# Optimization experiments

Hardware: AMD Instinct MI355X
Metric: run time of the kernel (lower is better)

Reference implementation:

```python
import jax, jax.numpy as jnp
import numpy as np

# Static 4-level feature pyramid (H, W) per level; total tokens = 20197
SHAPES = [(100, 152), (50, 76), (25, 38), (13, 19)]
B, S, E, H, L, P, R = 4, 1024, 256, 8, 4, 20, 4
HD = E // H
OFFSET_SCALE = 4.0


def setup_inputs() -> dict:
    key = jax.random.key(0)
    ks = jax.random.split(key, 11)
    total = sum(h * w for h, w in SHAPES)
    s = 0.02
    return {
        "x": jax.random.normal(ks[0], (B, S, E), jnp.float32),
        "encoder_input": jax.random.normal(ks[1], (B, total, E), jnp.float32),
        "v_w": jax.random.normal(ks[2], (E, E), jnp.float32) * s,
        "out_w": jax.random.normal(ks[3], (E, E), jnp.float32) * s,
        "off_w": jax.random.normal(ks[4], (H * L * P * 2, E), jnp.float32) * s,
        "off_b": jax.random.normal(ks[5], (H * L * P * 2,), jnp.float32) * s,
        "attn_w": jax.random.normal(ks[6], (H * L * P, E), jnp.float32) * s,
        "attn_b": jax.random.normal(ks[7], (H * L * P,), jnp.float32) * s,
        "ref_w": jax.random.normal(ks[8], (H * R, E), jnp.float32) * s,
        "ref_b": jax.random.normal(ks[9], (H * R,), jnp.float32) * s,
        "def_refs": jax.random.uniform(ks[10], (R, 2), jnp.float32, 0.1, 0.9),
        "spatial_shapes": jnp.array(SHAPES, dtype=jnp.int32),
    }


def _grid_sample(img, gx, gy, Hh, Ww):
    """Bilinear grid_sample, padding_mode='zeros', align_corners=False.
    img: (N, C, Hh*Ww); gx, gy: (N, M) in [-1, 1]. Returns (N, C, M)."""
    x = ((gx + 1.0) * Ww - 1.0) * 0.5
    y = ((gy + 1.0) * Hh - 1.0) * 0.5
    x0 = jnp.floor(x)
    y0 = jnp.floor(y)
    wx = x - x0
    wy = y - y0
    x0i = x0.astype(jnp.int32)
    y0i = y0.astype(jnp.int32)
    N, C, _ = img.shape

    def gather(xi, yi):
        valid = (xi >= 0) & (xi < Ww) & (yi >= 0) & (yi < Hh)
        idx = jnp.clip(yi, 0, Hh - 1) * Ww + jnp.clip(xi, 0, Ww - 1)
        v = jnp.take_along_axis(
            img, jnp.broadcast_to(idx[:, None, :], (N, C, idx.shape[-1])), axis=2)
        return v * valid[:, None, :].astype(img.dtype)

    return (gather(x0i, y0i) * ((1 - wx) * (1 - wy))[:, None, :]
            + gather(x0i + 1, y0i) * (wx * (1 - wy))[:, None, :]
            + gather(x0i, y0i + 1) * ((1 - wx) * wy)[:, None, :]
            + gather(x0i + 1, y0i + 1) * (wx * wy)[:, None, :])


def reference(x, encoder_input, v_w, out_w, off_w, off_b, attn_w, attn_b,
              ref_w, ref_b, def_refs, spatial_shapes):
    b, s, _ = x.shape
    values = (encoder_input @ v_w.T).reshape(b, -1, H, HD)
    refs = jax.nn.sigmoid(def_refs)  # (R, 2), default reference points
    ref_mix = jax.nn.softmax((x @ ref_w.T + ref_b).reshape(b, s, H, R), axis=-1)
    anchors = jnp.einsum('bshr,rc->bshc', ref_mix, refs)  # (b, s, H, 2)
    offsets = (x @ off_w.T + off_b).reshape(b, s, H, L, P, 2)
    attn = jax.nn.softmax((x @ attn_w.T + attn_b).reshape(b, s, H, L * P),
                          axis=-1).reshape(b, s, H, L, P)

    out = jnp.zeros((b, s, H, HD), x.dtype)
    start = 0
    for lvl, (hh, ww) in enumerate(SHAPES):  # static per-level loop (L=4)
        img = values[:, start:start + hh * ww]  # (b, hh*ww, H, HD)
        start += hh * ww
        img = img.transpose(0, 2, 3, 1).reshape(b * H, HD, hh * ww)
        norm = jnp.array([max(ww, 1), max(hh, 1)], x.dtype)
        locs = anchors[:, :, :, None, :] + jnp.tanh(offsets[:, :, :, lvl]) * (OFFSET_SCALE / norm)
        grid = jnp.clip(locs, 0.0, 1.0) * 2.0 - 1.0  # (b, s, H, P, 2)
        grid = grid.transpose(0, 2, 1, 3, 4).reshape(b * H, s * P, 2)
        sampled = _grid_sample(img, grid[..., 0], grid[..., 1], hh, ww)  # (b*H, HD, s*P)
        sampled = sampled.reshape(b, H, HD, s, P)
        out = out + jnp.einsum('bhcsp,bshp->bshc', sampled, attn[:, :, :, lvl])
    return out.reshape(b, s, E) @ out_w.T
```

## Files before the change

kernel.cpp:

```cpp
#include <hip/hip_runtime.h>
#include <hip/hip_bf16.h>
#include <math.h>

#define NH 8
#define HD 32
#define EDIM 256
#define NL 4
#define NP 20
#define NR 4
#define SEQ 1024
#define BATCH 4
#define TOTAL 20197
#define OFF_SCALE 4.0f

#define M_ENC (BATCH * TOTAL)
#define M_PAD 80896
#define KDIM 256

typedef short bf16x8 __attribute__((ext_vector_type(8)));
typedef float f32x4  __attribute__((ext_vector_type(4)));

__global__ __launch_bounds__(256) void cast_f32_bf16_kernel(
    const float* __restrict__ src, unsigned short* __restrict__ dst,
    long n_src, long n_dst)
{
    long i = (long)blockIdx.x * blockDim.x + threadIdx.x;
    long stride = (long)gridDim.x * blockDim.x;
    for (long e = i * 8; e < n_dst; e += stride * 8) {
        unsigned short o[8];
        if (e < n_src) {
            float4 a = *reinterpret_cast<const float4*>(src + e);
            float4 b = *reinterpret_cast<const float4*>(src + e + 4);
            float f[8] = {a.x, a.y, a.z, a.w, b.x, b.y, b.z, b.w};
            #pragma unroll
            for (int j = 0; j < 8; ++j) {
                unsigned u = __float_as_uint(f[j]);
                o[j] = (unsigned short)((u + 0x7fffu + ((u >> 16) & 1u)) >> 16);
            }
        } else {
            #pragma unroll
            for (int j = 0; j < 8; ++j) o[j] = 0;
        }
        *reinterpret_cast<uint4*>(dst + e) = *reinterpret_cast<const uint4*>(o);
    }
}

__global__ __launch_bounds__(256) void gemm_mfma_kernel(
    const unsigned short* __restrict__ A,
    const unsigned short* __restrict__ W,
    const float* __restrict__ bias,
    float* __restrict__ C,
    int M_real, int N)
{
    __shared__ __align__(16) unsigned short As[128 * 32];
    __shared__ __align__(16) unsigned short Ws[128 * 32];

    const int tid  = threadIdx.x;
    const int m0   = blockIdx.x * 128;
    const int n0   = blockIdx.y * 128;
    const int wave = tid >> 6;
    const int lane = tid & 63;
    const int wr   = wave >> 1;
    const int wc   = wave & 1;
    const int lrow = lane & 15;
    const int kg   = lane >> 4;

    f32x4 acc[4][4] = {};

    const bf16x8* Asv = reinterpret_cast<const bf16x8*>(As);
    const bf16x8* Wsv = reinterpret_cast<const bf16x8*>(Ws);

    for (int k0 = 0; k0 < KDIM; k0 += 32) {
        #pragma unroll
        for (int it = 0; it < 2; ++it) {
            int s   = tid + it * 256;
            int row = s >> 2;
            int ks  = s & 3;
            uint4 va = *reinterpret_cast<const uint4*>(A + (size_t)(m0 + row) * KDIM + k0 + ks * 8);
            uint4 vw = *reinterpret_cast<const uint4*>(W + (size_t)(n0 + row) * KDIM + k0 + ks * 8);
            *reinterpret_cast<uint4*>(&As[s * 8]) = va;
            *reinterpret_cast<uint4*>(&Ws[s * 8]) = vw;
        }
        __syncthreads();

        bf16x8 af[4], bfr[4];
        #pragma unroll
        for (int mi = 0; mi < 4; ++mi)
            af[mi] = Asv[(wr * 64 + mi * 16 + lrow) * 4 + kg];
        #pragma unroll
        for (int nj = 0; nj < 4; ++nj)
            bfr[nj] = Wsv[(wc * 64 + nj * 16 + lrow) * 4 + kg];
        #pragma unroll
        for (int mi = 0; mi < 4; ++mi)
            #pragma unroll
            for (int nj = 0; nj < 4; ++nj)
                acc[mi][nj] = __builtin_amdgcn_mfma_f32_16x16x32_bf16(
                    af[mi], bfr[nj], acc[mi][nj], 0, 0, 0);
        __syncthreads();
    }

    #pragma unroll
    for (int mi = 0; mi < 4; ++mi) {
        #pragma unroll
        for (int nj = 0; nj < 4; ++nj) {
            int row_base = m0 + wr * 64 + mi * 16 + kg * 4;
            int col      = n0 + wc * 64 + nj * 16 + lrow;
            float bv = bias ? bias[col] : 0.f;
            #pragma unroll
            for (int r = 0; r < 4; ++r) {
                int row = row_base + r;
                if (row < M_real)
                    C[(size_t)row * N + col] = acc[mi][nj][r] + bv;
            }
        }
    }
}

__global__ __launch_bounds__(256) void gemm_atb_kernel(
    const float* __restrict__ A, const float* __restrict__ W,
    const float* __restrict__ bias, float* __restrict__ C,
    int M, int N, int K)
{
    __shared__ float As[16][64];
    __shared__ float Wt[16][64];

    const int tid = threadIdx.x;
    const int m0 = blockIdx.x * 64;
    const int n0 = blockIdx.y * 64;
    const int tx = tid & 15;
    const int ty = tid >> 4;
    const int lr = tid >> 2;
    const int lk = (tid & 3) << 2;

    const int am = m0 + lr;
    const int wn = n0 + lr;

    float acc[4][4] = {};

    for (int k0 = 0; k0 < K; k0 += 16) {
        float4 av = make_float4(0.f, 0.f, 0.f, 0.f);
        float4 wv = make_float4(0.f, 0.f, 0.f, 0.f);
        if (am < M) av = *reinterpret_cast<const float4*>(&A[(size_t)am * K + k0 + lk]);
        if (wn < N) wv = *reinterpret_cast<const float4*>(&W[(size_t)wn * K + k0 + lk]);
        As[lk + 0][lr] = av.x; As[lk + 1][lr] = av.y;
        As[lk + 2][lr] = av.z; As[lk + 3][lr] = av.w;
        Wt[lk + 0][lr] = wv.x; Wt[lk + 1][lr] = wv.y;
        Wt[lk + 2][lr] = wv.z; Wt[lk + 3][lr] = wv.w;
        __syncthreads();

        #pragma unroll
        for (int k = 0; k < 16; ++k) {
            float a[4], b[4];
            #pragma unroll
            for (int i = 0; i < 4; ++i) a[i] = As[k][ty * 4 + i];
            #pragma unroll
            for (int j = 0; j < 4; ++j) b[j] = Wt[k][tx * 4 + j];
            #pragma unroll
            for (int i = 0; i < 4; ++i)
                #pragma unroll
                for (int j = 0; j < 4; ++j)
                    acc[i][j] += a[i] * b[j];
        }
        __syncthreads();
    }

    #pragma unroll
    for (int i = 0; i < 4; ++i) {
        int m = m0 + ty * 4 + i;
        if (m >= M) continue;
        #pragma unroll
        for (int j = 0; j < 4; ++j) {
            int n = n0 + tx * 4 + j;
            if (n >= N) continue;
            float v = acc[i][j];
            if (bias) v += bias[n];
            C[(size_t)m * N + n] = v;
        }
    }
}

__global__ __launch_bounds__(256) void deform_sample_kernel(
    const float* __restrict__ values,
    const float* __restrict__ proj_off,
    const float* __restrict__ proj_attn,
    const float* __restrict__ proj_ref,
    const float* __restrict__ def_refs,
    float* __restrict__ out)
{
    const int row = blockIdx.x;
    const int b   = row >> 10;
    const int tid = threadIdx.x;

    __shared__ float  attn_s[NH * NL * NP];
    __shared__ float  anchors[NH][2];
    __shared__ unsigned int sidx[NH * NL * NP][2];
    __shared__ float4 wcor[NH * NL * NP];

    if (tid >= 96) {
        int i = tid - 96;
        reinterpret_cast<float4*>(attn_s)[i] =
            reinterpret_cast<const float4*>(proj_attn + (size_t)row * 640)[i];
    } else if (tid < NH) {
        const int h = tid;
        float rv[NR];
        float rmax = -1e30f;
        #pragma unroll
        for (int r = 0; r < NR; ++r) {
            rv[r] = proj_ref[(size_t)row * (NH * NR) + h * NR + r];
            rmax = fmaxf(rmax, rv[r]);
        }
        float rsum = 0.f;
        #pragma unroll
        for (int r = 0; r < NR; ++r) { rv[r] = __expf(rv[r] - rmax); rsum += rv[r]; }
        float ax = 0.f, ay = 0.f;
        #pragma unroll
        for (int r = 0; r < NR; ++r) {
            float pr = rv[r] / rsum;
            float sx = 1.f / (1.f + __expf(-def_refs[r * 2 + 0]));
            float sy = 1.f / (1.f + __expf(-def_refs[r * 2 + 1]));
            ax += pr * sx; ay += pr * sy;
        }
        anchors[h][0] = ax; anchors[h][1] = ay;
    }
    __syncthreads();

    {
        const int g = tid >> 5;
        const int l = tid & 31;
        float v0 = attn_s[g * 80 + l];
        float v1 = attn_s[g * 80 + 32 + l];
        float v2 = (l < 16) ? attn_s[g * 80 + 64 + l] : -1e30f;
        float m = fmaxf(fmaxf(v0, v1), v2);
        #pragma unroll
        for (int d = 16; d >= 1; d >>= 1) m = fmaxf(m, __shfl_xor(m, d, 64));
        float e0 = __expf(v0 - m), e1 = __expf(v1 - m);
        float e2 = (l < 16) ? __expf(v2 - m) : 0.f;
        float s = e0 + e1 + e2;
        #pragma unroll
        for (int d = 16; d >= 1; d >>= 1) s += __shfl_xor(s, d, 64);
        float inv = 1.f / s;
        __syncthreads();
        attn_s[g * 80 + l]      = e0 * inv;
        attn_s[g * 80 + 32 + l] = e1 * inv;
        if (l < 16) attn_s[g * 80 + 64 + l] = e2 * inv;
    }
    __syncthreads();

    const int lhh[NL] = {100, 50, 25, 13};
    const int lww[NL] = {152, 76, 38, 19};
    const int lst[NL] = {0, 15200, 19000, 19950};

    for (int e = tid; e < NH * NL * NP; e += 256) {
        int h = e / 80;
        int rem = e - h * 80;
        int l = rem / 20;
        const float2 o = *reinterpret_cast<const float2*>(
            proj_off + (size_t)row * 1280 + e * 2);
        float offx = tanhf(o.x);
        float offy = tanhf(o.y);
        int ww = lww[l], hh = lhh[l];
        float locx = fminf(fmaxf(anchors[h][0] + offx * (OFF_SCALE / (float)ww), 0.f), 1.f);
        float locy = fminf(fmaxf(anchors[h][1] + offy * (OFF_SCALE / (float)hh), 0.f), 1.f);
        float xx = locx * (float)ww - 0.5f;
        float yy = locy * (float)hh - 0.5f;
        float x0f = floorf(xx), y0f = floorf(yy);
        int x0 = (int)x0f, y0 = (int)y0f;
        float wx = xx - x0f, wy = yy - y0f;
        float wa = attn_s[e];

        float bx0 = (x0 >= 0)      ? 1.f : 0.f;
        float bx1 = (x0 < ww - 1)  ? 1.f : 0.f;
        float by0 = (y0 >= 0)      ? 1.f : 0.f;
        float by1 = (y0 < hh - 1)  ? 1.f : 0.f;
        int xc0 = max(x0, 0), xc1 = min(x0 + 1, ww - 1);
        int yc0 = max(y0, 0), yc1 = min(y0 + 1, hh - 1);
        unsigned int i00 = (unsigned int)(lst[l] + yc0 * ww + xc0);
        unsigned int i10 = (unsigned int)(lst[l] + yc0 * ww + xc1);
        unsigned int i01 = (unsigned int)(lst[l] + yc1 * ww + xc0);
        unsigned int i11 = (unsigned int)(lst[l] + yc1 * ww + xc1);

        float4 w;
        w.x = wa * (1.f - wx) * (1.f - wy) * bx0 * by0;
        w.y = wa * wx * (1.f - wy) * bx1 * by0;
        w.z = wa * (1.f - wx) * wy * bx0 * by1;
        w.w = wa * wx * wy * bx1 * by1;

        sidx[e][0] = i00 | (i10 << 16);
        sidx[e][1] = i01 | (i11 << 16);
        wcor[e] = w;
    }
    __syncthreads();

    const int h = tid >> 5;
    const int c = tid & 31;
    const float* vb = values + (size_t)b * TOTAL * 256 + h * 32 + c;
    float acc = 0.f;
    #pragma unroll 4
    for (int i = 0; i < 80; ++i) {
        int e = h * 80 + i;
        unsigned int p0 = sidx[e][0];
        unsigned int p1 = sidx[e][1];
        float4 w = wcor[e];
        float v00 = vb[(size_t)(p0 & 0xffffu) * 256];
        float v10 = vb[(size_t)(p0 >> 16) * 256];
        float v01 = vb[(size_t)(p1 & 0xffffu) * 256];
        float v11 = vb[(size_t)(p1 >> 16) * 256];
        acc += w.x * v00 + w.y * v10 + w.z * v01 + w.w * v11;
    }
    out[(size_t)row * 256 + h * 32 + c] = acc;
}

extern "C" void kernel_launch(void* const* d_in, const int* in_sizes, int n_in,
                              void* d_out, int out_size, void* d_ws, size_t ws_size,
                              hipStream_t stream)
{
    const float* x        = (const float*)d_in[0];
    const float* enc      = (const float*)d_in[1];
    const float* v_w      = (const float*)d_in[2];
    const float* out_w    = (const float*)d_in[3];
    const float* off_w    = (const float*)d_in[4];
    const float* off_b    = (const float*)d_in[5];
    const float* attn_w   = (const float*)d_in[6];
    const float* attn_b   = (const float*)d_in[7];
    const float* ref_w    = (const float*)d_in[8];
    const float* ref_b    = (const float*)d_in[9];
    const float* def_refs = (const float*)d_in[10];
    float* out = (float*)d_out;

    const int M_Q    = BATCH * SEQ;
    const int N_OFF  = NH * NL * NP * 2;
    const int N_ATTN = NH * NL * NP;
    const int N_REF  = NH * NR;

    float* ws = (float*)d_ws;
    float* values = ws;
    char*  region2 = (char*)(values + (size_t)M_ENC * EDIM);
    unsigned short* enc_bf16 = (unsigned short*)region2;
    float* proj_off  = (float*)region2;
    float* proj_attn = proj_off  + (size_t)M_Q * N_OFF;
    float* proj_ref  = proj_attn + (size_t)M_Q * N_ATTN;
    float* attn_out  = proj_ref  + (size_t)M_Q * N_REF;
    unsigned short* x_bf16     = (unsigned short*)(attn_out + (size_t)M_Q * EDIM);
    unsigned short* offw_bf16  = x_bf16 + (size_t)M_Q * KDIM;
    unsigned short* attnw_bf16 = offw_bf16 + (size_t)N_OFF * KDIM;
    unsigned short* vw_bf16    = (unsigned short*)(region2 + (size_t)M_PAD * KDIM * 2);

    dim3 blk(256);

    cast_f32_bf16_kernel<<<dim3(2048), blk, 0, stream>>>(
        enc, enc_bf16, (long)M_ENC * EDIM, (long)M_PAD * KDIM);
    cast_f32_bf16_kernel<<<dim3(64), blk, 0, stream>>>(
        v_w, vw_bf16, (long)EDIM * EDIM, (long)EDIM * EDIM);

    gemm_mfma_kernel<<<dim3(M_PAD / 128, EDIM / 128), blk, 0, stream>>>(
        enc_bf16, vw_bf16, nullptr, values, M_ENC, EDIM);

    cast_f32_bf16_kernel<<<dim3(512), blk, 0, stream>>>(
        x, x_bf16, (long)M_Q * EDIM, (long)M_Q * EDIM);
    cast_f32_bf16_kernel<<<dim3(160), blk, 0, stream>>>(
        off_w, offw_bf16, (long)N_OFF * EDIM, (long)N_OFF * EDIM);
    cast_f32_bf16_kernel<<<dim3(40), blk, 0, stream>>>(
        attn_w, attnw_bf16, (long)N_ATTN * EDIM, (long)N_ATTN * EDIM);

    gemm_mfma_kernel<<<dim3(M_Q / 128, N_OFF / 128), blk, 0, stream>>>(
        x_bf16, offw_bf16, off_b, proj_off, M_Q, N_OFF);
    gemm_mfma_kernel<<<dim3(M_Q / 128, N_ATTN / 128), blk, 0, stream>>>(
        x_bf16, attnw_bf16, attn_b, proj_attn, M_Q, N_ATTN);
    gemm_atb_kernel<<<dim3(M_Q / 64, 1), blk, 0, stream>>>(
        x, ref_w, ref_b, proj_ref, M_Q, N_REF, EDIM);

    deform_sample_kernel<<<dim3(M_Q), blk, 0, stream>>>(
        values, proj_off, proj_attn, proj_ref, def_refs, attn_out);

    gemm_atb_kernel<<<dim3(M_Q / 64, EDIM / 64), blk, 0, stream>>>(
        attn_out, out_w, nullptr, out, M_Q, EDIM, EDIM);
}
```

Baseline: 319.5 us.

## Fuse activation f32-to-bf16 cast into GEMM A-tile loads and pad LDS rows

```diff
diff --git a/kernel.cpp b/kernel.cpp
--- a/kernel.cpp
+++ b/kernel.cpp
@@ -14,46 +14,43 @@
 #define OFF_SCALE 4.0f
 
 #define M_ENC (BATCH * TOTAL)
-#define M_PAD 80896
 #define KDIM 256
+#define LDSW 40
 
 typedef short bf16x8 __attribute__((ext_vector_type(8)));
 typedef float f32x4  __attribute__((ext_vector_type(4)));
 
+__device__ __forceinline__ unsigned short f32_to_bf16_rne(float f) {
+    unsigned u = __float_as_uint(f);
+    return (unsigned short)((u + 0x7fffu + ((u >> 16) & 1u)) >> 16);
+}
+
 __global__ __launch_bounds__(256) void cast_f32_bf16_kernel(
     const float* __restrict__ src, unsigned short* __restrict__ dst,
-    long n_src, long n_dst)
+    long n)
 {
     long i = (long)blockIdx.x * blockDim.x + threadIdx.x;
     long stride = (long)gridDim.x * blockDim.x;
-    for (long e = i * 8; e < n_dst; e += stride * 8) {
+    for (long e = i * 8; e < n; e += stride * 8) {
+        float4 a = *reinterpret_cast<const float4*>(src + e);
+        float4 b = *reinterpret_cast<const float4*>(src + e + 4);
+        float f[8] = {a.x, a.y, a.z, a.w, b.x, b.y, b.z, b.w};
         unsigned short o[8];
-        if (e < n_src) {
-            float4 a = *reinterpret_cast<const float4*>(src + e);
-            float4 b = *reinterpret_cast<const float4*>(src + e + 4);
-            float f[8] = {a.x, a.y, a.z, a.w, b.x, b.y, b.z, b.w};
-            #pragma unroll
-            for (int j = 0; j < 8; ++j) {
-                unsigned u = __float_as_uint(f[j]);
-                o[j] = (unsigned short)((u + 0x7fffu + ((u >> 16) & 1u)) >> 16);
-            }
-        } else {
-            #pragma unroll
-            for (int j = 0; j < 8; ++j) o[j] = 0;
-        }
+        #pragma unroll
+        for (int j = 0; j < 8; ++j) o[j] = f32_to_bf16_rne(f[j]);
         *reinterpret_cast<uint4*>(dst + e) = *reinterpret_cast<const uint4*>(o);
     }
 }
 
-__global__ __launch_bounds__(256) void gemm_mfma_kernel(
-    const unsigned short* __restrict__ A,
+__global__ __launch_bounds__(256) void gemm_mfma_f32a_kernel(
+    const float* __restrict__ A,
     const unsigned short* __restrict__ W,
     const float* __restrict__ bias,
     float* __restrict__ C,
     int M_real, int N)
 {
-    __shared__ __align__(16) unsigned short As[128 * 32];
-    __shared__ __align__(16) unsigned short Ws[128 * 32];
+    __shared__ __align__(16) unsigned short As[128 * LDSW];
+    __shared__ __align__(16) unsigned short Ws[128 * LDSW];
 
     const int tid  = threadIdx.x;
     const int m0   = blockIdx.x * 128;
@@ -67,29 +64,42 @@
 
     f32x4 acc[4][4] = {};
 
-    const bf16x8* Asv = reinterpret_cast<const bf16x8*>(As);
-    const bf16x8* Wsv = reinterpret_cast<const bf16x8*>(Ws);
-
     for (int k0 = 0; k0 < KDIM; k0 += 32) {
+        #pragma unroll
+        for (int p = 0; p < 4; ++p) {
+            int s   = tid + p * 256;
+            int row = s >> 3;
+            int sl  = s & 7;
+            int gm  = m0 + row;
+            float4 v = make_float4(0.f, 0.f, 0.f, 0.f);
+            if (gm < M_real)
+                v = *reinterpret_cast<const float4*>(&A[(size_t)gm * KDIM + k0 + sl * 4]);
+            unsigned short o[4] = {
+                f32_to_bf16_rne(v.x), f32_to_bf16_rne(v.y),
+                f32_to_bf16_rne(v.z), f32_to_bf16_rne(v.w)};
+            *reinterpret_cast<uint2*>(&As[row * LDSW + sl * 4]) =
+                *reinterpret_cast<const uint2*>(o);
+        }
         #pragma unroll
         for (int it = 0; it < 2; ++it) {
             int s   = tid + it * 256;
             int row = s >> 2;
             int ks  = s & 3;
-            uint4 va = *reinterpret_cast<const uint4*>(A + (size_t)(m0 + row) * KDIM + k0 + ks * 8);
-            uint4 vw = *reinterpret_cast<const uint4*>(W + (size_t)(n0 + row) * KDIM + k0 + ks * 8);
-            *reinterpret_cast<uint4*>(&As[s * 8]) = va;
-            *reinterpret_cast<uint4*>(&Ws[s * 8]) = vw;
+            uint4 vw = *reinterpret_cast<const uint4*>(
+                W + (size_t)(n0 + row) * KDIM + k0 + ks * 8);
+            *reinterpret_cast<uint4*>(&Ws[row * LDSW + ks * 8]) = vw;
         }
         __syncthreads();
 
         bf16x8 af[4], bfr[4];
         #pragma unroll
         for (int mi = 0; mi < 4; ++mi)
-            af[mi] = Asv[(wr * 64 + mi * 16 + lrow) * 4 + kg];
+            af[mi] = *reinterpret_cast<const bf16x8*>(
+                &As[(wr * 64 + mi * 16 + lrow) * LDSW + kg * 8]);
         #pragma unroll
         for (int nj = 0; nj < 4; ++nj)
-            bfr[nj] = Wsv[(wc * 64 + nj * 16 + lrow) * 4 + kg];
+            bfr[nj] = *reinterpret_cast<const bf16x8*>(
+                &Ws[(wc * 64 + nj * 16 + lrow) * LDSW + kg * 8]);
         #pragma unroll
         for (int mi = 0; mi < 4; ++mi)
             #pragma unroll
@@ -333,39 +343,28 @@
     const int N_REF  = NH * NR;
 
     float* ws = (float*)d_ws;
-    float* values = ws;
-    char*  region2 = (char*)(values + (size_t)M_ENC * EDIM);
-    unsigned short* enc_bf16 = (unsigned short*)region2;
-    float* proj_off  = (float*)region2;
+    float* values    = ws;
+    float* proj_off  = values    + (size_t)M_ENC * EDIM;
     float* proj_attn = proj_off  + (size_t)M_Q * N_OFF;
     float* proj_ref  = proj_attn + (size_t)M_Q * N_ATTN;
     float* attn_out  = proj_ref  + (size_t)M_Q * N_REF;
-    unsigned short* x_bf16     = (unsigned short*)(attn_out + (size_t)M_Q * EDIM);
-    unsigned short* offw_bf16  = x_bf16 + (size_t)M_Q * KDIM;
+    unsigned short* vw_bf16    = (unsigned short*)(attn_out + (size_t)M_Q * EDIM);
+    unsigned short* offw_bf16  = vw_bf16   + (size_t)EDIM * KDIM;
     unsigned short* attnw_bf16 = offw_bf16 + (size_t)N_OFF * KDIM;
-    unsigned short* vw_bf16    = (unsigned short*)(region2 + (size_t)M_PAD * KDIM * 2);
 
     dim3 blk(256);
 
-    cast_f32_bf16_kernel<<<dim3(2048), blk, 0, stream>>>(
-        enc, enc_bf16, (long)M_ENC * EDIM, (long)M_PAD * KDIM);
-    cast_f32_bf16_kernel<<<dim3(64), blk, 0, stream>>>(
-        v_w, vw_bf16, (long)EDIM * EDIM, (long)EDIM * EDIM);
-
-    gemm_mfma_kernel<<<dim3(M_PAD / 128, EDIM / 128), blk, 0, stream>>>(
-        enc_bf16, vw_bf16, nullptr, values, M_ENC, EDIM);
-
-    cast_f32_bf16_kernel<<<dim3(512), blk, 0, stream>>>(
-        x, x_bf16, (long)M_Q * EDIM, (long)M_Q * EDIM);
-    cast_f32_bf16_kernel<<<dim3(160), blk, 0, stream>>>(
-        off_w, offw_bf16, (long)N_OFF * EDIM, (long)N_OFF * EDIM);
-    cast_f32_bf16_kernel<<<dim3(40), blk, 0, stream>>>(
-        attn_w, attnw_bf16, (long)N_ATTN * EDIM, (long)N_ATTN * EDIM);
-
-    gemm_mfma_kernel<<<dim3(M_Q / 128, N_OFF / 128), blk, 0, stream>>>(
-        x_bf16, offw_bf16, off_b, proj_off, M_Q, N_OFF);
-    gemm_mfma_kernel<<<dim3(M_Q / 128, N_ATTN / 128), blk, 0, stream>>>(
-        x_bf16, attnw_bf16, attn_b, proj_attn, M_Q, N_ATTN);
+    cast_f32_bf16_kernel<<<dim3(32), blk, 0, stream>>>(v_w, vw_bf16, (long)EDIM * KDIM);
+    cast_f32_bf16_kernel<<<dim3(160), blk, 0, stream>>>(off_w, offw_bf16, (long)N_OFF * KDIM);
+    cast_f32_bf16_kernel<<<dim3(80), blk, 0, stream>>>(attn_w, attnw_bf16, (long)N_ATTN * KDIM);
+
+    gemm_mfma_f32a_kernel<<<dim3((M_ENC + 127) / 128, EDIM / 128), blk, 0, stream>>>(
+        enc, vw_bf16, nullptr, values, M_ENC, EDIM);
+
+    gemm_mfma_f32a_kernel<<<dim3(M_Q / 128, N_OFF / 128), blk, 0, stream>>>(
+        x, offw_bf16, off_b, proj_off, M_Q, N_OFF);
+    gemm_mfma_f32a_kernel<<<dim3(M_Q / 128, N_ATTN / 128), blk, 0, stream>>>(
+        x, attnw_bf16, attn_b, proj_attn, M_Q, N_ATTN);
     gemm_atb_kernel<<<dim3(M_Q / 64, 1), blk, 0, stream>>>(
         x, ref_w, ref_b, proj_ref, M_Q, N_REF, EDIM);
 
```

Measured after the change: 334.6 us. 4.7% more time.
